# Performance work log

Measured on AMD Instinct MI355X. Metric: run time of the kernel, lower is better.

The kernel has to match this reference:

```python
import jax, jax.numpy as jnp
import numpy as np

# SamplesLoss(loss='sinkhorn', p=1, blur=0.05): entropic regularization eps = blur**p = 0.05,
# debiased Sinkhorn divergence S(a,b) = OT(a,b) - 0.5*OT(a,a) - 0.5*OT(b,b).
EPS = 0.05
N_ITER = 50
N_POINTS = 32


def _cost(X, Y):
    # p=1 cost: Euclidean distance. X:[B,N,D] Y:[B,M,D] -> [B,N,M]
    d2 = jnp.sum((X[:, :, None, :] - Y[:, None, :, :]) ** 2, axis=-1)
    return jnp.sqrt(d2 + 1e-12)


def _ot(X, Y):
    # log-domain Sinkhorn with uniform weights; returns dual cost <mu,f>+<nu,g> per batch.
    B, N, _ = X.shape
    M = Y.shape[1]
    C = _cost(X, Y)  # [B,N,M]
    log_mu = jnp.full((B, N), -np.log(N), C.dtype)
    log_nu = jnp.full((B, M), -np.log(M), C.dtype)

    def body(carry, _):
        f, g = carry
        f = -EPS * jax.nn.logsumexp((g[:, None, :] - C) / EPS + log_nu[:, None, :], axis=2)
        g = -EPS * jax.nn.logsumexp((f[:, :, None] - C) / EPS + log_mu[:, :, None], axis=1)
        return (f, g), None

    init = (jnp.zeros((B, N), C.dtype), jnp.zeros((B, M), C.dtype))
    (f, g), _ = jax.lax.scan(body, init, None, length=N_ITER)
    return jnp.mean(f, axis=-1) + jnp.mean(g, axis=-1)  # uniform weights => mean


def _sinkhorn_div(X, Y):
    return _ot(X, Y) - 0.5 * _ot(X, X) - 0.5 * _ot(Y, Y)


def _encode(x, W, edge_index):
    # simple 1-layer GCN-style encoder: linear + mean neighbor aggregation + self, ReLU
    h = x @ W  # [n_nodes, emb_dim]
    src, dst = edge_index[0], edge_index[1]
    n = x.shape[0]
    agg = jax.ops.segment_sum(h[src], dst, num_segments=n)
    deg = jax.ops.segment_sum(jnp.ones(src.shape, h.dtype), dst, num_segments=n)
    return jax.nn.relu(h + agg / jnp.maximum(deg, 1.0)[:, None])


def setup_inputs() -> dict:
    key = jax.random.key(0)
    k1, k2, k3, k4, k5 = jax.random.split(key, 5)
    n_nodes, d_feat, emb_dim = 50000, 128, 256
    n_edges, n_pairs = 800000, 8192
    x = jax.random.normal(k1, (n_nodes, d_feat), jnp.float32)
    W = jax.random.normal(k2, (d_feat, emb_dim), jnp.float32) / np.sqrt(d_feat)
    edge_index = jax.random.randint(k3, (2, n_edges), 0, n_nodes, jnp.int64)
    pairs = jax.random.randint(k4, (2, n_pairs), 0, n_nodes, jnp.int64)
    graph_dist = jax.random.uniform(k5, (n_pairs,), jnp.float32, 1.0, 5.0)
    return {"x": x, "W": W, "edge_index": edge_index, "pairs": pairs,
            "graph_dist": graph_dist}


def reference(x, W, edge_index, pairs, graph_dist):
    z = _encode(x, W, edge_index)                       # [n_nodes, emb_dim]
    B = pairs.shape[1]
    Xa = z[pairs[0]].reshape(B, N_POINTS, -1)           # [B, n_points, space_dim]
    Xb = z[pairs[1]].reshape(B, N_POINTS, -1)
    distance = _sinkhorn_div(Xa, Xb)                    # = -score_pairs
    distortion = jnp.abs(distance - graph_dist) / graph_dist
    return jnp.mean(distortion)
```

## Files before the change

### kernel.cpp

```cpp
#include <hip/hip_runtime.h>

#define N_NODES 50000
#define N_EDGES 800000
#define N_PAIRS 8192
#define N_SLOTS (2 * N_PAIRS)
#define CAP     64

#define INV_EPS   20.0f
#define LOG2E_F   1.4426950408889634f
#define LN2_F     0.6931471805599453f
#define LN32_F    3.4657359027997265f
#define EPS_F     0.05f

typedef float f2 __attribute__((ext_vector_type(2)));

__global__ void k_mark(const int* __restrict__ pairs, int* __restrict__ flags) {
    int t = blockIdx.x * 256 + threadIdx.x;
    if (t < N_SLOTS) flags[pairs[t]] = 1;
}

__global__ __launch_bounds__(256) void k_scatter(
        const int* __restrict__ eidx, const int* __restrict__ flags,
        int* __restrict__ cnt, int* __restrict__ bucket) {
    int t = blockIdx.x * 256 + threadIdx.x;
    int dst = eidx[N_EDGES + t];
    if (!flags[dst]) return;
    int pos = atomicAdd(&cnt[dst], 1);
    if (pos < CAP) bucket[dst * CAP + pos] = eidx[t];
}

__global__ __launch_bounds__(256) void k_gemm(
        const int* __restrict__ pairs, const float* __restrict__ x,
        const int* __restrict__ cnt, const int* __restrict__ bucket,
        const float* __restrict__ W, float* __restrict__ Z) {
    __shared__ __align__(16) float Us[16 * 128];
    int sbase = blockIdx.x * 16;
    int t = threadIdx.x;
    int wave = t >> 6, lane = t & 63;

    #pragma unroll
    for (int rr = 0; rr < 4; ++rr) {
        int r = wave * 4 + rr;
        int node = pairs[sbase + r];
        int n = cnt[node];
        int m = (n < CAP) ? n : CAP;
        const int* bk = bucket + node * CAP;
        float ax = 0.0f, ay = 0.0f;
        int k = 0;
        for (; k + 4 <= m; k += 4) {
            int s0 = bk[k], s1 = bk[k + 1], s2 = bk[k + 2], s3 = bk[k + 3];
            float2 v0 = *(const float2*)(x + (size_t)s0 * 128 + lane * 2);
            float2 v1 = *(const float2*)(x + (size_t)s1 * 128 + lane * 2);
            float2 v2 = *(const float2*)(x + (size_t)s2 * 128 + lane * 2);
            float2 v3 = *(const float2*)(x + (size_t)s3 * 128 + lane * 2);
            ax += (v0.x + v1.x) + (v2.x + v3.x);
            ay += (v0.y + v1.y) + (v2.y + v3.y);
        }
        for (; k < m; ++k) {
            int s0 = bk[k];
            float2 v0 = *(const float2*)(x + (size_t)s0 * 128 + lane * 2);
            ax += v0.x;
            ay += v0.y;
        }
        float rdeg = 1.0f / fmaxf((float)n, 1.0f);
        float2 xv = *(const float2*)(x + (size_t)node * 128 + lane * 2);
        float2 o;
        o.x = fmaf(ax, rdeg, xv.x);
        o.y = fmaf(ay, rdeg, xv.y);
        *(float2*)(Us + r * 128 + lane * 2) = o;
    }
    __syncthreads();

    int jq = t & 63;
    int rq = t >> 6;
    float acc[4][4] = {};
    const float4* Wv = (const float4*)W;

    for (int k4 = 0; k4 < 32; ++k4) {
        float4 wv[4];
        #pragma unroll
        for (int i = 0; i < 4; ++i) wv[i] = Wv[(size_t)(k4 * 4 + i) * 64 + jq];
        #pragma unroll
        for (int r = 0; r < 4; ++r) {
            float4 uv = *(const float4*)(Us + (rq * 4 + r) * 128 + k4 * 4);
            float uk0 = uv.x, uk1 = uv.y, uk2 = uv.z, uk3 = uv.w;
            acc[r][0] = fmaf(uk0, wv[0].x, acc[r][0]);
            acc[r][1] = fmaf(uk0, wv[0].y, acc[r][1]);
            acc[r][2] = fmaf(uk0, wv[0].z, acc[r][2]);
            acc[r][3] = fmaf(uk0, wv[0].w, acc[r][3]);
            acc[r][0] = fmaf(uk1, wv[1].x, acc[r][0]);
            acc[r][1] = fmaf(uk1, wv[1].y, acc[r][1]);
            acc[r][2] = fmaf(uk1, wv[1].z, acc[r][2]);
            acc[r][3] = fmaf(uk1, wv[1].w, acc[r][3]);
            acc[r][0] = fmaf(uk2, wv[2].x, acc[r][0]);
            acc[r][1] = fmaf(uk2, wv[2].y, acc[r][1]);
            acc[r][2] = fmaf(uk2, wv[2].z, acc[r][2]);
            acc[r][3] = fmaf(uk2, wv[2].w, acc[r][3]);
            acc[r][0] = fmaf(uk3, wv[3].x, acc[r][0]);
            acc[r][1] = fmaf(uk3, wv[3].y, acc[r][1]);
            acc[r][2] = fmaf(uk3, wv[3].z, acc[r][2]);
            acc[r][3] = fmaf(uk3, wv[3].w, acc[r][3]);
        }
    }

    #pragma unroll
    for (int r = 0; r < 4; ++r) {
        float4 o;
        o.x = fmaxf(acc[r][0], 0.0f);
        o.y = fmaxf(acc[r][1], 0.0f);
        o.z = fmaxf(acc[r][2], 0.0f);
        o.w = fmaxf(acc[r][3], 0.0f);
        *(float4*)(Z + (size_t)(sbase + rq * 4 + r) * 256 + jq * 4) = o;
    }
}

__global__ __launch_bounds__(128) void k_sinkhorn(
        const float* __restrict__ Z, float* __restrict__ dist) {
    __shared__ __align__(16) float smem[2][1280];

    int w = threadIdx.x >> 6;
    int lane = threadIdx.x & 63;
    float* S = &smem[w][0];
    const float CSCALE = -INV_EPS * LOG2E_F;
    const float CBIAS  = -LN32_F * LOG2E_F;

    if (blockIdx.x < 4096) {
        int h = lane >> 5, i = lane & 31;
        int q = (i >> 4) & 1;
        int ip = i ^ 16;
        int P = blockIdx.x * 2 + w;
        int src = h ? (N_PAIRS + P) : P;

        float* sP  = S + h * 256;
        float* swv = S + 512;
        float* spv = S + 576;

        {
            const float4* zp = (const float4*)(Z + (size_t)src * 256);
            *(float4*)(&sP[i * 8])     = zp[i * 2];
            *(float4*)(&sP[i * 8 + 4]) = zp[i * 2 + 1];
        }

        f2 CA[8], CB[8];
        {
            const f2* xp = (const f2*)(&sP[i * 8]);
            f2 x0 = xp[0], x1 = xp[1], x2 = xp[2], x3 = xp[3];
            const f2* bp = (const f2*)(&sP[ip * 8]);
            f2 b0 = bp[0], b1 = bp[1], b2 = bp[2], b3 = bp[3];
            #pragma unroll
            for (int t = 0; t < 16; ++t) {
                int j = q * 16 + t;
                const f2* yp = (const f2*)(&sP[j * 8]);
                f2 y0 = yp[0], y1 = yp[1], y2 = yp[2], y3 = yp[3];
                f2 d, s2;
                d = x0 - y0; s2 = d * d;
                d = x1 - y1; s2 = __builtin_elementwise_fma(d, d, s2);
                d = x2 - y2; s2 = __builtin_elementwise_fma(d, d, s2);
                d = x3 - y3; s2 = __builtin_elementwise_fma(d, d, s2);
                float d2 = s2.x + s2.y + 1e-12f;
                CA[t >> 1][t & 1] = fmaf(__builtin_amdgcn_sqrtf(d2), CSCALE, CBIAS);
                d = b0 - y0; s2 = d * d;
                d = b1 - y1; s2 = __builtin_elementwise_fma(d, d, s2);
                d = b2 - y2; s2 = __builtin_elementwise_fma(d, d, s2);
                d = b3 - y3; s2 = __builtin_elementwise_fma(d, d, s2);
                float e2 = s2.x + s2.y + 1e-12f;
                CB[t >> 1][t & 1] = fmaf(__builtin_amdgcn_sqrtf(e2), CSCALE, CBIAS);
            }
        }

        float pp = 0.0f, E = 1.0f, wcur = 1.0f, wprev = 1.0f;
        f2 KA[8], KB[8];
        #pragma unroll
        for (int t = 0; t < 8; ++t) {
            KA[t].x = __builtin_amdgcn_exp2f(CA[t].x);
            KA[t].y = __builtin_amdgcn_exp2f(CA[t].y);
            KB[t].x = __builtin_amdgcn_exp2f(CB[t].x);
            KB[t].y = __builtin_amdgcn_exp2f(CB[t].y);
        }
        swv[lane] = 1.0f;

        const int blens[9] = {4, 12, 12, 12, 12, 12, 12, 12, 12};
        #pragma unroll 1
        for (int blk = 0; blk < 9; ++blk) {
            int L = blens[blk];
            #pragma unroll 2
            for (int s = 0; s < L; ++s) {
                const float4* wp = (const float4*)(&swv[h * 32 + q * 16]);
                float4 A0 = wp[0], A1 = wp[1], A2 = wp[2], A3 = wp[3];
                f2 aA0 = KA[0] * f2{A0.x, A0.y};
                f2 aA1 = KA[1] * f2{A0.z, A0.w};
                f2 aB0 = KB[0] * f2{A0.x, A0.y};
                f2 aB1 = KB[1] * f2{A0.z, A0.w};
                aA0 = __builtin_elementwise_fma(KA[2], f2{A1.x, A1.y}, aA0);
                aA1 = __builtin_elementwise_fma(KA[3], f2{A1.z, A1.w}, aA1);
                aB0 = __builtin_elementwise_fma(KB[2], f2{A1.x, A1.y}, aB0);
                aB1 = __builtin_elementwise_fma(KB[3], f2{A1.z, A1.w}, aB1);
                aA0 = __builtin_elementwise_fma(KA[4], f2{A2.x, A2.y}, aA0);
                aA1 = __builtin_elementwise_fma(KA[5], f2{A2.z, A2.w}, aA1);
                aB0 = __builtin_elementwise_fma(KB[4], f2{A2.x, A2.y}, aB0);
                aB1 = __builtin_elementwise_fma(KB[5], f2{A2.z, A2.w}, aB1);
                aA0 = __builtin_elementwise_fma(KA[6], f2{A3.x, A3.y}, aA0);
                aA1 = __builtin_elementwise_fma(KA[7], f2{A3.z, A3.w}, aA1);
                aB0 = __builtin_elementwise_fma(KB[6], f2{A3.x, A3.y}, aB0);
                aB1 = __builtin_elementwise_fma(KB[7], f2{A3.z, A3.w}, aB1);
                f2 aa = aA0 + aA1;
                f2 bb = aB0 + aB1;
                float pa = aa.x + aa.y;
                float pb = bb.x + bb.y;
                float other = __shfl_xor(pb, 16);
                float Sv = pa + other;
                wprev = wcur;
                wcur = __builtin_amdgcn_rcpf(Sv) * E;
                swv[h * 32 + i] = wcur;
            }
            if (blk < 8) {
                float d = __builtin_amdgcn_logf(wcur);
                pp += d;
                spv[h * 32 + i] = d;
                const float4* dv = (const float4*)(&spv[h * 32 + q * 16]);
                float4 D0 = dv[0], D1 = dv[1], D2 = dv[2], D3 = dv[3];
                float ex[16];
                ex[0]  = __builtin_amdgcn_exp2f(D0.x);
                ex[1]  = __builtin_amdgcn_exp2f(D0.y);
                ex[2]  = __builtin_amdgcn_exp2f(D0.z);
                ex[3]  = __builtin_amdgcn_exp2f(D0.w);
                ex[4]  = __builtin_amdgcn_exp2f(D1.x);
                ex[5]  = __builtin_amdgcn_exp2f(D1.y);
                ex[6]  = __builtin_amdgcn_exp2f(D1.z);
                ex[7]  = __builtin_amdgcn_exp2f(D1.w);
                ex[8]  = __builtin_amdgcn_exp2f(D2.x);
                ex[9]  = __builtin_amdgcn_exp2f(D2.y);
                ex[10] = __builtin_amdgcn_exp2f(D2.z);
                ex[11] = __builtin_amdgcn_exp2f(D2.w);
                ex[12] = __builtin_amdgcn_exp2f(D3.x);
                ex[13] = __builtin_amdgcn_exp2f(D3.y);
                ex[14] = __builtin_amdgcn_exp2f(D3.z);
                ex[15] = __builtin_amdgcn_exp2f(D3.w);
                #pragma unroll
                for (int t2 = 0; t2 < 8; ++t2) {
                    f2 ee = f2{ex[2 * t2], ex[2 * t2 + 1]};
                    KA[t2] *= ee;
                    KB[t2] *= ee;
                }
                E = __builtin_amdgcn_exp2f(-pp);
                wcur = 1.0f;
                swv[lane] = 1.0f;
            }
        }

        float zsum = 2.0f * pp + __builtin_amdgcn_logf(wprev)
                   + __builtin_amdgcn_logf(wcur);
        #pragma unroll
        for (int off = 16; off > 0; off >>= 1) zsum += __shfl_xor(zsum, off);
        if (i == 0) {
            float cost = zsum * (EPS_F * LN2_F / 32.0f);
            unsafeAtomicAdd(&dist[P], -0.5f * cost);
        }
    } else {
        int h = lane >> 5, l = lane & 31;
        int p = (blockIdx.x - 4096) * 4 + w * 2 + h;

        float* base = S + h * 640;
        float* sX = base;
        float* sY = base + 256;
        float* sf = base + 512;
        float* sg = base + 544;
        float* su = base + 576;
        float* sv = base + 608;

        {
            const float4* zx = (const float4*)(Z + (size_t)p * 256);
            const float4* zy = (const float4*)(Z + (size_t)(N_PAIRS + p) * 256);
            *(float4*)(&sX[l * 8])     = zx[l * 2];
            *(float4*)(&sX[l * 8 + 4]) = zx[l * 2 + 1];
            *(float4*)(&sY[l * 8])     = zy[l * 2];
            *(float4*)(&sY[l * 8 + 4]) = zy[l * 2 + 1];
        }
        sg[l] = 0.0f;

        f2 Crow[16], Ccol[16];
        {
            const f2* xp = (const f2*)(&sX[l * 8]);
            f2 x0 = xp[0], x1 = xp[1], x2 = xp[2], x3 = xp[3];
            const f2* yp = (const f2*)(&sY[l * 8]);
            f2 y0 = yp[0], y1 = yp[1], y2 = yp[2], y3 = yp[3];
            #pragma unroll
            for (int t = 0; t < 32; ++t) {
                const f2* op = (const f2*)(&sY[t * 8]);
                f2 d, s2;
                d = x0 - op[0]; s2 = d * d;
                d = x1 - op[1]; s2 = __builtin_elementwise_fma(d, d, s2);
                d = x2 - op[2]; s2 = __builtin_elementwise_fma(d, d, s2);
                d = x3 - op[3]; s2 = __builtin_elementwise_fma(d, d, s2);
                float d2 = s2.x + s2.y + 1e-12f;
                Crow[t >> 1][t & 1] = fmaf(__builtin_amdgcn_sqrtf(d2), CSCALE, CBIAS);
                const f2* qp = (const f2*)(&sX[t * 8]);
                d = qp[0] - y0; s2 = d * d;
                d = qp[1] - y1; s2 = __builtin_elementwise_fma(d, d, s2);
                d = qp[2] - y2; s2 = __builtin_elementwise_fma(d, d, s2);
                d = qp[3] - y3; s2 = __builtin_elementwise_fma(d, d, s2);
                float e2 = s2.x + s2.y + 1e-12f;
                Ccol[t >> 1][t & 1] = fmaf(__builtin_amdgcn_sqrtf(e2), CSCALE, CBIAS);
            }
        }

        float ft = 0.0f, gt = 0.0f;

        #pragma unroll 1
        for (int it = 0; it < 2; ++it) {
            {
                const float4* gp = (const float4*)sg;
                float4 G[8];
                #pragma unroll
                for (int r = 0; r < 8; ++r) G[r] = gp[r];
                f2 val[16], m2 = f2{-1e30f, -1e30f};
                #pragma unroll
                for (int r = 0; r < 8; ++r) {
                    val[2 * r]     = f2{G[r].x, G[r].y} + Crow[2 * r];
                    val[2 * r + 1] = f2{G[r].z, G[r].w} + Crow[2 * r + 1];
                    m2 = __builtin_elementwise_max(m2, val[2 * r]);
                    m2 = __builtin_elementwise_max(m2, val[2 * r + 1]);
                }
                float m = fmaxf(m2.x, m2.y);
                f2 mm = f2{m, m};
                float s0 = 0.0f, s1 = 0.0f;
                #pragma unroll
                for (int t2 = 0; t2 < 16; ++t2) {
                    f2 e = val[t2] - mm;
                    s0 += __builtin_amdgcn_exp2f(e.x);
                    s1 += __builtin_amdgcn_exp2f(e.y);
                }
                ft = -(m + __builtin_amdgcn_logf(s0 + s1));
            }
            sf[l] = ft;
            {
                const float4* fp = (const float4*)sf;
                float4 F[8];
                #pragma unroll
                for (int r = 0; r < 8; ++r) F[r] = fp[r];
                f2 val[16], m2 = f2{-1e30f, -1e30f};
                #pragma unroll
                for (int r = 0; r < 8; ++r) {
                    val[2 * r]     = f2{F[r].x, F[r].y} + Ccol[2 * r];
                    val[2 * r + 1] = f2{F[r].z, F[r].w} + Ccol[2 * r + 1];
                    m2 = __builtin_elementwise_max(m2, val[2 * r]);
                    m2 = __builtin_elementwise_max(m2, val[2 * r + 1]);
                }
                float m = fmaxf(m2.x, m2.y);
                f2 mm = f2{m, m};
                float s0 = 0.0f, s1 = 0.0f;
                #pragma unroll
                for (int t2 = 0; t2 < 16; ++t2) {
                    f2 e = val[t2] - mm;
                    s0 += __builtin_amdgcn_exp2f(e.x);
                    s1 += __builtin_amdgcn_exp2f(e.y);
                }
                gt = -(m + __builtin_amdgcn_logf(s0 + s1));
            }
            sg[l] = gt;
        }

        f2 KR[16], KC[16];
        {
            const float4* gp = (const float4*)sg;
            #pragma unroll
            for (int r = 0; r < 8; ++r) {
                float4 G = gp[r];
                f2 a0 = f2{G.x, G.y} + Crow[2 * r] + f2{ft, ft};
                f2 a1 = f2{G.z, G.w} + Crow[2 * r + 1] + f2{ft, ft};
                KR[2 * r].x     = __builtin_amdgcn_exp2f(a0.x);
                KR[2 * r].y     = __builtin_amdgcn_exp2f(a0.y);
                KR[2 * r + 1].x = __builtin_amdgcn_exp2f(a1.x);
                KR[2 * r + 1].y = __builtin_amdgcn_exp2f(a1.y);
            }
            const float4* fp = (const float4*)sf;
            #pragma unroll
            for (int r = 0; r < 8; ++r) {
                float4 F = fp[r];
                f2 a0 = f2{F.x, F.y} + Ccol[2 * r] + f2{gt, gt};
                f2 a1 = f2{F.z, F.w} + Ccol[2 * r + 1] + f2{gt, gt};
                KC[2 * r].x     = __builtin_amdgcn_exp2f(a0.x);
                KC[2 * r].y     = __builtin_amdgcn_exp2f(a0.y);
                KC[2 * r + 1].x = __builtin_amdgcn_exp2f(a1.x);
                KC[2 * r + 1].y = __builtin_amdgcn_exp2f(a1.y);
            }
        }
        sv[l] = 1.0f;
        float ureg = 1.0f, vreg = 1.0f;

        const int blens[5] = {6, 6, 12, 12, 12};
        #pragma unroll 1
        for (int blk = 0; blk < 5; ++blk) {
            int L = blens[blk];
            #pragma unroll 2
            for (int s6 = 0; s6 < L; ++s6) {
                {
                    const float4* vp = (const float4*)sv;
                    f2 acc0, acc1;
                    float4 A = vp[0];
                    acc0 = KR[0] * f2{A.x, A.y};
                    acc1 = KR[1] * f2{A.z, A.w};
                    #pragma unroll
                    for (int r = 1; r < 8; ++r) {
                        float4 B = vp[r];
                        acc0 = __builtin_elementwise_fma(KR[2 * r],     f2{B.x, B.y}, acc0);
                        acc1 = __builtin_elementwise_fma(KR[2 * r + 1], f2{B.z, B.w}, acc1);
                    }
                    f2 a = acc0 + acc1;
                    ureg = __builtin_amdgcn_rcpf(a.x + a.y);
                }
                su[l] = ureg;
                {
                    const float4* up = (const float4*)su;
                    f2 acc0, acc1;
                    float4 A = up[0];
                    acc0 = KC[0] * f2{A.x, A.y};
                    acc1 = KC[1] * f2{A.z, A.w};
                    #pragma unroll
                    for (int r = 1; r < 8; ++r) {
                        float4 B = up[r];
                        acc0 = __builtin_elementwise_fma(KC[2 * r],     f2{B.x, B.y}, acc0);
                        acc1 = __builtin_elementwise_fma(KC[2 * r + 1], f2{B.z, B.w}, acc1);
                    }
                    f2 a = acc0 + acc1;
                    vreg = __builtin_amdgcn_rcpf(a.x + a.y);
                }
                sv[l] = vreg;
            }
            if (blk < 4) {
                float df = __builtin_amdgcn_logf(ureg);
                float dg = __builtin_amdgcn_logf(vreg);
                ft += df;
                gt += dg;
                sf[l] = df;
                sg[l] = dg;
                const float4* dgv = (const float4*)sg;
                #pragma unroll
                for (int r = 0; r < 8; ++r) {
                    float4 D = dgv[r];
                    f2 e0, e1;
                    e0.x = __builtin_amdgcn_exp2f(df + D.x);
                    e0.y = __builtin_amdgcn_exp2f(df + D.y);
                    e1.x = __builtin_amdgcn_exp2f(df + D.z);
                    e1.y = __builtin_amdgcn_exp2f(df + D.w);
                    KR[2 * r]     *= e0;
                    KR[2 * r + 1] *= e1;
                }
                const float4* dfv = (const float4*)sf;
                #pragma unroll
                for (int r = 0; r < 8; ++r) {
                    float4 D = dfv[r];
                    f2 e0, e1;
                    e0.x = __builtin_amdgcn_exp2f(dg + D.x);
                    e0.y = __builtin_amdgcn_exp2f(dg + D.y);
                    e1.x = __builtin_amdgcn_exp2f(dg + D.z);
                    e1.y = __builtin_amdgcn_exp2f(dg + D.w);
                    KC[2 * r]     *= e0;
                    KC[2 * r + 1] *= e1;
                }
                sv[l] = 1.0f;
                ureg = 1.0f;
                vreg = 1.0f;
            }
        }
        ft += __builtin_amdgcn_logf(ureg);
        gt += __builtin_amdgcn_logf(vreg);

        float v = ft + gt;
        #pragma unroll
        for (int off = 16; off > 0; off >>= 1) v += __shfl_xor(v, off);
        if (l == 0) {
            float cost = v * (EPS_F * LN2_F / 32.0f);
            unsafeAtomicAdd(&dist[p], cost);
        }
    }
}

__global__ void k_finalize(const float* __restrict__ dist,
                           const float* __restrict__ gd, float* __restrict__ out) {
    __shared__ float red[256];
    float s = 0.0f;
    for (int i = threadIdx.x; i < N_PAIRS; i += 256) {
        float g = gd[i];
        s += fabsf(dist[i] - g) / g;
    }
    red[threadIdx.x] = s;
    __syncthreads();
    for (int o = 128; o > 0; o >>= 1) {
        if (threadIdx.x < o) red[threadIdx.x] += red[threadIdx.x + o];
        __syncthreads();
    }
    if (threadIdx.x == 0) out[0] = red[0] * (1.0f / N_PAIRS);
}

extern "C" void kernel_launch(void* const* d_in, const int* in_sizes, int n_in,
                              void* d_out, int out_size, void* d_ws, size_t ws_size,
                              hipStream_t stream) {
    const float* x    = (const float*)d_in[0];
    const float* W    = (const float*)d_in[1];
    const int*   eidx = (const int*)d_in[2];
    const int*   pair = (const int*)d_in[3];
    const float* gd   = (const float*)d_in[4];

    char* ws = (char*)d_ws;
    size_t off = 0;
    int*   cnt    = (int*)  (ws + off); off += (size_t)N_NODES * 4;
    int*   flags  = (int*)  (ws + off); off += (size_t)N_NODES * 4;
    float* dist   = (float*)(ws + off); off += (size_t)N_PAIRS * 4;
    size_t zero_bytes = off;
    int*   bucket = (int*)  (ws + off); off += (size_t)N_NODES * CAP * 4;
    float* Z      = (float*)(ws + off); off += (size_t)N_SLOTS * 256 * 4;

    hipMemsetAsync(d_ws, 0, zero_bytes, stream);
    k_mark    <<<(N_SLOTS + 255) / 256, 256, 0, stream>>>(pair, flags);
    k_scatter <<<N_EDGES / 256, 256, 0, stream>>>(eidx, flags, cnt, bucket);
    k_gemm    <<<N_SLOTS / 16, 256, 0, stream>>>(pair, x, cnt, bucket, W, Z);
    k_sinkhorn<<<6144, 128, 0, stream>>>(Z, dist);
    k_finalize<<<1, 256, 0, stream>>>(dist, gd, (float*)d_out);
}
```

Measured before the change: 244.0 us.

## Process two symmetric Sinkhorn pairs per wavefront to interleave independent iterations

Each wavefront in the symmetric (OT(a,a)/OT(b,b)) branch now handles two pairs at once, interleaving their Sinkhorn matrix-vector updates so the two independent dependency chains can hide each other's LDS, shuffle and rcp latency. The grid for that branch halves, reducing the total block count from 6144 to 4096. The exp2 of the cost is also folded into the kernel build loop. This doubles register use for the kernel matrices, which may lower occupancy, and leaves fewer waves to spread across the GPU.

Measured after the change: 242.3 us. Within noise of the previous version (-0.7%).

```diff
diff --git a/kernel.cpp b/kernel.cpp
--- a/kernel.cpp
+++ b/kernel.cpp
@@ -124,33 +124,36 @@
     const float CSCALE = -INV_EPS * LOG2E_F;
     const float CBIAS  = -LN32_F * LOG2E_F;
 
-    if (blockIdx.x < 4096) {
+    if (blockIdx.x < 2048) {
         int h = lane >> 5, i = lane & 31;
         int q = (i >> 4) & 1;
         int ip = i ^ 16;
-        int P = blockIdx.x * 2 + w;
-        int src = h ? (N_PAIRS + P) : P;
-
-        float* sP  = S + h * 256;
-        float* swv = S + 512;
-        float* spv = S + 576;
-
-        {
-            const float4* zp = (const float4*)(Z + (size_t)src * 256);
-            *(float4*)(&sP[i * 8])     = zp[i * 2];
-            *(float4*)(&sP[i * 8 + 4]) = zp[i * 2 + 1];
-        }
-
-        f2 CA[8], CB[8];
-        {
-            const f2* xp = (const f2*)(&sP[i * 8]);
+        int P0 = blockIdx.x * 4 + w * 2;
+
+        float* sP   = S;
+        float* swv0 = S + 512;
+        float* spv0 = S + 576;
+        float* swv1 = S + 640;
+        float* spv1 = S + 704;
+
+        f2 KA0[8], KB0[8], KA1[8], KB1[8];
+
+        auto build = [&](f2 (&KA)[8], f2 (&KB)[8], int P) {
+            int src = h ? (N_PAIRS + P) : P;
+            float* sPh = sP + h * 256;
+            {
+                const float4* zp = (const float4*)(Z + (size_t)src * 256);
+                *(float4*)(&sPh[i * 8])     = zp[i * 2];
+                *(float4*)(&sPh[i * 8 + 4]) = zp[i * 2 + 1];
+            }
+            const f2* xp = (const f2*)(&sPh[i * 8]);
             f2 x0 = xp[0], x1 = xp[1], x2 = xp[2], x3 = xp[3];
-            const f2* bp = (const f2*)(&sP[ip * 8]);
+            const f2* bp = (const f2*)(&sPh[ip * 8]);
             f2 b0 = bp[0], b1 = bp[1], b2 = bp[2], b3 = bp[3];
             #pragma unroll
             for (int t = 0; t < 16; ++t) {
                 int j = q * 16 + t;
-                const f2* yp = (const f2*)(&sP[j * 8]);
+                const f2* yp = (const f2*)(&sPh[j * 8]);
                 f2 y0 = yp[0], y1 = yp[1], y2 = yp[2], y3 = yp[3];
                 f2 d, s2;
                 d = x0 - y0; s2 = d * d;
@@ -158,107 +161,170 @@
                 d = x2 - y2; s2 = __builtin_elementwise_fma(d, d, s2);
                 d = x3 - y3; s2 = __builtin_elementwise_fma(d, d, s2);
                 float d2 = s2.x + s2.y + 1e-12f;
-                CA[t >> 1][t & 1] = fmaf(__builtin_amdgcn_sqrtf(d2), CSCALE, CBIAS);
+                KA[t >> 1][t & 1] = __builtin_amdgcn_exp2f(
+                    fmaf(__builtin_amdgcn_sqrtf(d2), CSCALE, CBIAS));
                 d = b0 - y0; s2 = d * d;
                 d = b1 - y1; s2 = __builtin_elementwise_fma(d, d, s2);
                 d = b2 - y2; s2 = __builtin_elementwise_fma(d, d, s2);
                 d = b3 - y3; s2 = __builtin_elementwise_fma(d, d, s2);
                 float e2 = s2.x + s2.y + 1e-12f;
-                CB[t >> 1][t & 1] = fmaf(__builtin_amdgcn_sqrtf(e2), CSCALE, CBIAS);
-            }
-        }
-
-        float pp = 0.0f, E = 1.0f, wcur = 1.0f, wprev = 1.0f;
-        f2 KA[8], KB[8];
-        #pragma unroll
-        for (int t = 0; t < 8; ++t) {
-            KA[t].x = __builtin_amdgcn_exp2f(CA[t].x);
-            KA[t].y = __builtin_amdgcn_exp2f(CA[t].y);
-            KB[t].x = __builtin_amdgcn_exp2f(CB[t].x);
-            KB[t].y = __builtin_amdgcn_exp2f(CB[t].y);
-        }
-        swv[lane] = 1.0f;
+                KB[t >> 1][t & 1] = __builtin_amdgcn_exp2f(
+                    fmaf(__builtin_amdgcn_sqrtf(e2), CSCALE, CBIAS));
+            }
+        };
+        build(KA0, KB0, P0);
+        build(KA1, KB1, P0 + 1);
+
+        float pp0 = 0.0f, pp1 = 0.0f, E0 = 1.0f, E1 = 1.0f;
+        float w0c = 1.0f, w0p = 1.0f, w1c = 1.0f, w1p = 1.0f;
+        swv0[lane] = 1.0f;
+        swv1[lane] = 1.0f;
 
         const int blens[9] = {4, 12, 12, 12, 12, 12, 12, 12, 12};
         #pragma unroll 1
         for (int blk = 0; blk < 9; ++blk) {
             int L = blens[blk];
-            #pragma unroll 2
+            #pragma unroll 1
             for (int s = 0; s < L; ++s) {
-                const float4* wp = (const float4*)(&swv[h * 32 + q * 16]);
-                float4 A0 = wp[0], A1 = wp[1], A2 = wp[2], A3 = wp[3];
-                f2 aA0 = KA[0] * f2{A0.x, A0.y};
-                f2 aA1 = KA[1] * f2{A0.z, A0.w};
-                f2 aB0 = KB[0] * f2{A0.x, A0.y};
-                f2 aB1 = KB[1] * f2{A0.z, A0.w};
-                aA0 = __builtin_elementwise_fma(KA[2], f2{A1.x, A1.y}, aA0);
-                aA1 = __builtin_elementwise_fma(KA[3], f2{A1.z, A1.w}, aA1);
-                aB0 = __builtin_elementwise_fma(KB[2], f2{A1.x, A1.y}, aB0);
-                aB1 = __builtin_elementwise_fma(KB[3], f2{A1.z, A1.w}, aB1);
-                aA0 = __builtin_elementwise_fma(KA[4], f2{A2.x, A2.y}, aA0);
-                aA1 = __builtin_elementwise_fma(KA[5], f2{A2.z, A2.w}, aA1);
-                aB0 = __builtin_elementwise_fma(KB[4], f2{A2.x, A2.y}, aB0);
-                aB1 = __builtin_elementwise_fma(KB[5], f2{A2.z, A2.w}, aB1);
-                aA0 = __builtin_elementwise_fma(KA[6], f2{A3.x, A3.y}, aA0);
-                aA1 = __builtin_elementwise_fma(KA[7], f2{A3.z, A3.w}, aA1);
-                aB0 = __builtin_elementwise_fma(KB[6], f2{A3.x, A3.y}, aB0);
-                aB1 = __builtin_elementwise_fma(KB[7], f2{A3.z, A3.w}, aB1);
-                f2 aa = aA0 + aA1;
-                f2 bb = aB0 + aB1;
-                float pa = aa.x + aa.y;
-                float pb = bb.x + bb.y;
-                float other = __shfl_xor(pb, 16);
-                float Sv = pa + other;
-                wprev = wcur;
-                wcur = __builtin_amdgcn_rcpf(Sv) * E;
-                swv[h * 32 + i] = wcur;
+                const float4* wp0 = (const float4*)(&swv0[h * 32 + q * 16]);
+                const float4* wp1 = (const float4*)(&swv1[h * 32 + q * 16]);
+                float4 A0 = wp0[0], A1 = wp0[1], A2 = wp0[2], A3 = wp0[3];
+                float4 B0 = wp1[0], B1 = wp1[1], B2 = wp1[2], B3 = wp1[3];
+                f2 aA0 = KA0[0] * f2{A0.x, A0.y};
+                f2 aA1 = KA0[1] * f2{A0.z, A0.w};
+                f2 aB0 = KB0[0] * f2{A0.x, A0.y};
+                f2 aB1 = KB0[1] * f2{A0.z, A0.w};
+                aA0 = __builtin_elementwise_fma(KA0[2], f2{A1.x, A1.y}, aA0);
+                aA1 = __builtin_elementwise_fma(KA0[3], f2{A1.z, A1.w}, aA1);
+                aB0 = __builtin_elementwise_fma(KB0[2], f2{A1.x, A1.y}, aB0);
+                aB1 = __builtin_elementwise_fma(KB0[3], f2{A1.z, A1.w}, aB1);
+                aA0 = __builtin_elementwise_fma(KA0[4], f2{A2.x, A2.y}, aA0);
+                aA1 = __builtin_elementwise_fma(KA0[5], f2{A2.z, A2.w}, aA1);
+                aB0 = __builtin_elementwise_fma(KB0[4], f2{A2.x, A2.y}, aB0);
+                aB1 = __builtin_elementwise_fma(KB0[5], f2{A2.z, A2.w}, aB1);
+                aA0 = __builtin_elementwise_fma(KA0[6], f2{A3.x, A3.y}, aA0);
+                aA1 = __builtin_elementwise_fma(KA0[7], f2{A3.z, A3.w}, aA1);
+                aB0 = __builtin_elementwise_fma(KB0[6], f2{A3.x, A3.y}, aB0);
+                aB1 = __builtin_elementwise_fma(KB0[7], f2{A3.z, A3.w}, aB1);
+                f2 aa0 = aA0 + aA1;
+                f2 bb0 = aB0 + aB1;
+                float pa0 = aa0.x + aa0.y;
+                float pb0 = bb0.x + bb0.y;
+                f2 cA0 = KA1[0] * f2{B0.x, B0.y};
+                f2 cA1 = KA1[1] * f2{B0.z, B0.w};
+                f2 cB0 = KB1[0] * f2{B0.x, B0.y};
+                f2 cB1 = KB1[1] * f2{B0.z, B0.w};
+                cA0 = __builtin_elementwise_fma(KA1[2], f2{B1.x, B1.y}, cA0);
+                cA1 = __builtin_elementwise_fma(KA1[3], f2{B1.z, B1.w}, cA1);
+                cB0 = __builtin_elementwise_fma(KB1[2], f2{B1.x, B1.y}, cB0);
+                cB1 = __builtin_elementwise_fma(KB1[3], f2{B1.z, B1.w}, cB1);
+                cA0 = __builtin_elementwise_fma(KA1[4], f2{B2.x, B2.y}, cA0);
+                cA1 = __builtin_elementwise_fma(KA1[5], f2{B2.z, B2.w}, cA1);
+                cB0 = __builtin_elementwise_fma(KB1[4], f2{B2.x, B2.y}, cB0);
+                cB1 = __builtin_elementwise_fma(KB1[5], f2{B2.z, B2.w}, cB1);
+                cA0 = __builtin_elementwise_fma(KA1[6], f2{B3.x, B3.y}, cA0);
+                cA1 = __builtin_elementwise_fma(KA1[7], f2{B3.z, B3.w}, cA1);
+                cB0 = __builtin_elementwise_fma(KB1[6], f2{B3.x, B3.y}, cB0);
+                cB1 = __builtin_elementwise_fma(KB1[7], f2{B3.z, B3.w}, cB1);
+                f2 aa1 = cA0 + cA1;
+                f2 bb1 = cB0 + cB1;
+                float pa1 = aa1.x + aa1.y;
+                float pb1 = bb1.x + bb1.y;
+                float o0 = __shfl_xor(pb0, 16);
+                float o1 = __shfl_xor(pb1, 16);
+                w0p = w0c;
+                w0c = __builtin_amdgcn_rcpf(pa0 + o0) * E0;
+                w1p = w1c;
+                w1c = __builtin_amdgcn_rcpf(pa1 + o1) * E1;
+                swv0[h * 32 + i] = w0c;
+                swv1[h * 32 + i] = w1c;
             }
             if (blk < 8) {
-                float d = __builtin_amdgcn_logf(wcur);
-                pp += d;
-                spv[h * 32 + i] = d;
-                const float4* dv = (const float4*)(&spv[h * 32 + q * 16]);
-                float4 D0 = dv[0], D1 = dv[1], D2 = dv[2], D3 = dv[3];
-                float ex[16];
-                ex[0]  = __builtin_amdgcn_exp2f(D0.x);
-                ex[1]  = __builtin_amdgcn_exp2f(D0.y);
-                ex[2]  = __builtin_amdgcn_exp2f(D0.z);
-                ex[3]  = __builtin_amdgcn_exp2f(D0.w);
-                ex[4]  = __builtin_amdgcn_exp2f(D1.x);
-                ex[5]  = __builtin_amdgcn_exp2f(D1.y);
-                ex[6]  = __builtin_amdgcn_exp2f(D1.z);
-                ex[7]  = __builtin_amdgcn_exp2f(D1.w);
-                ex[8]  = __builtin_amdgcn_exp2f(D2.x);
-                ex[9]  = __builtin_amdgcn_exp2f(D2.y);
-                ex[10] = __builtin_amdgcn_exp2f(D2.z);
-                ex[11] = __builtin_amdgcn_exp2f(D2.w);
-                ex[12] = __builtin_amdgcn_exp2f(D3.x);
-                ex[13] = __builtin_amdgcn_exp2f(D3.y);
-                ex[14] = __builtin_amdgcn_exp2f(D3.z);
-                ex[15] = __builtin_amdgcn_exp2f(D3.w);
-                #pragma unroll
-                for (int t2 = 0; t2 < 8; ++t2) {
-                    f2 ee = f2{ex[2 * t2], ex[2 * t2 + 1]};
-                    KA[t2] *= ee;
-                    KB[t2] *= ee;
-                }
-                E = __builtin_amdgcn_exp2f(-pp);
-                wcur = 1.0f;
-                swv[lane] = 1.0f;
-            }
-        }
-
-        float zsum = 2.0f * pp + __builtin_amdgcn_logf(wprev)
-                   + __builtin_amdgcn_logf(wcur);
+                float d0 = __builtin_amdgcn_logf(w0c);
+                float d1 = __builtin_amdgcn_logf(w1c);
+                pp0 += d0;
+                pp1 += d1;
+                spv0[h * 32 + i] = d0;
+                spv1[h * 32 + i] = d1;
+                {
+                    const float4* dv = (const float4*)(&spv0[h * 32 + q * 16]);
+                    float4 D0 = dv[0], D1 = dv[1], D2 = dv[2], D3 = dv[3];
+                    float ex[16];
+                    ex[0]  = __builtin_amdgcn_exp2f(D0.x);
+                    ex[1]  = __builtin_amdgcn_exp2f(D0.y);
+                    ex[2]  = __builtin_amdgcn_exp2f(D0.z);
+                    ex[3]  = __builtin_amdgcn_exp2f(D0.w);
+                    ex[4]  = __builtin_amdgcn_exp2f(D1.x);
+                    ex[5]  = __builtin_amdgcn_exp2f(D1.y);
+                    ex[6]  = __builtin_amdgcn_exp2f(D1.z);
+                    ex[7]  = __builtin_amdgcn_exp2f(D1.w);
+                    ex[8]  = __builtin_amdgcn_exp2f(D2.x);
+                    ex[9]  = __builtin_amdgcn_exp2f(D2.y);
+                    ex[10] = __builtin_amdgcn_exp2f(D2.z);
+                    ex[11] = __builtin_amdgcn_exp2f(D2.w);
+                    ex[12] = __builtin_amdgcn_exp2f(D3.x);
+                    ex[13] = __builtin_amdgcn_exp2f(D3.y);
+                    ex[14] = __builtin_amdgcn_exp2f(D3.z);
+                    ex[15] = __builtin_amdgcn_exp2f(D3.w);
+                    #pragma unroll
+                    for (int t2 = 0; t2 < 8; ++t2) {
+                        f2 ee = f2{ex[2 * t2], ex[2 * t2 + 1]};
+                        KA0[t2] *= ee;
+                        KB0[t2] *= ee;
+                    }
+                }
+                {
+                    const float4* dv = (const float4*)(&spv1[h * 32 + q * 16]);
+                    float4 D0 = dv[0], D1 = dv[1], D2 = dv[2], D3 = dv[3];
+                    float ex[16];
+                    ex[0]  = __builtin_amdgcn_exp2f(D0.x);
+                    ex[1]  = __builtin_amdgcn_exp2f(D0.y);
+                    ex[2]  = __builtin_amdgcn_exp2f(D0.z);
+                    ex[3]  = __builtin_amdgcn_exp2f(D0.w);
+                    ex[4]  = __builtin_amdgcn_exp2f(D1.x);
+                    ex[5]  = __builtin_amdgcn_exp2f(D1.y);
+                    ex[6]  = __builtin_amdgcn_exp2f(D1.z);
+                    ex[7]  = __builtin_amdgcn_exp2f(D1.w);
+                    ex[8]  = __builtin_amdgcn_exp2f(D2.x);
+                    ex[9]  = __builtin_amdgcn_exp2f(D2.y);
+                    ex[10] = __builtin_amdgcn_exp2f(D2.z);
+                    ex[11] = __builtin_amdgcn_exp2f(D2.w);
+                    ex[12] = __builtin_amdgcn_exp2f(D3.x);
+                    ex[13] = __builtin_amdgcn_exp2f(D3.y);
+                    ex[14] = __builtin_amdgcn_exp2f(D3.z);
+                    ex[15] = __builtin_amdgcn_exp2f(D3.w);
+                    #pragma unroll
+                    for (int t2 = 0; t2 < 8; ++t2) {
+                        f2 ee = f2{ex[2 * t2], ex[2 * t2 + 1]};
+                        KA1[t2] *= ee;
+                        KB1[t2] *= ee;
+                    }
+                }
+                E0 = __builtin_amdgcn_exp2f(-pp0);
+                E1 = __builtin_amdgcn_exp2f(-pp1);
+                w0c = 1.0f;
+                w1c = 1.0f;
+                swv0[lane] = 1.0f;
+                swv1[lane] = 1.0f;
+            }
+        }
+
+        float zs0 = 2.0f * pp0 + __builtin_amdgcn_logf(w0p)
+                  + __builtin_amdgcn_logf(w0c);
+        float zs1 = 2.0f * pp1 + __builtin_amdgcn_logf(w1p)
+                  + __builtin_amdgcn_logf(w1c);
         #pragma unroll
-        for (int off = 16; off > 0; off >>= 1) zsum += __shfl_xor(zsum, off);
+        for (int off = 16; off > 0; off >>= 1) {
+            zs0 += __shfl_xor(zs0, off);
+            zs1 += __shfl_xor(zs1, off);
+        }
         if (i == 0) {
-            float cost = zsum * (EPS_F * LN2_F / 32.0f);
-            unsafeAtomicAdd(&dist[P], -0.5f * cost);
+            unsafeAtomicAdd(&dist[P0],     -0.5f * (zs0 * (EPS_F * LN2_F / 32.0f)));
+            unsafeAtomicAdd(&dist[P0 + 1], -0.5f * (zs1 * (EPS_F * LN2_F / 32.0f)));
         }
     } else {
         int h = lane >> 5, l = lane & 31;
-        int p = (blockIdx.x - 4096) * 4 + w * 2 + h;
+        int p = (blockIdx.x - 2048) * 4 + w * 2 + h;
 
         float* base = S + h * 640;
         float* sX = base;
@@ -515,6 +581,6 @@
     k_mark    <<<(N_SLOTS + 255) / 256, 256, 0, stream>>>(pair, flags);
     k_scatter <<<N_EDGES / 256, 256, 0, stream>>>(eidx, flags, cnt, bucket);
     k_gemm    <<<N_SLOTS / 16, 256, 0, stream>>>(pair, x, cnt, bucket, W, Z);
-    k_sinkhorn<<<6144, 128, 0, stream>>>(Z, dist);
+    k_sinkhorn<<<4096, 128, 0, stream>>>(Z, dist);
     k_finalize<<<1, 256, 0, stream>>>(dist, gd, (float*)d_out);
 }
```
